# Kernel optimization log

Hardware: AMD Instinct MI355X
Metric: run time of the kernel (lower is better)

Reference implementation:

```python
import jax, jax.numpy as jnp
import numpy as np

N = 20000          # num nodes
E = 320000         # num edges (avg degree 16)
IN = 128           # input feature dim
HID = 64           # layer1 out_channels per head
OUT = 128          # layer2 out_channels per head
H = 3              # attention heads
NEG = 0.15         # LeakyReLU negative slope
IN2 = IN + H * HID # layer2 input: concat(x, h1)


def setup_inputs() -> dict:
    key = jax.random.key(0)
    ks = jax.random.split(key, 12)
    lin = lambda k, fi, fo: (jax.random.normal(k, (fi, fo), jnp.float32) / np.float32(np.sqrt(fi)))
    return {
        "node_features": jax.random.normal(ks[0], (N, IN), jnp.float32),
        "Wl1": lin(ks[1], IN, H * HID),
        "bl1": jnp.zeros((H * HID,), jnp.float32),
        "Wr1": lin(ks[2], IN, H * HID),
        "br1": jnp.zeros((H * HID,), jnp.float32),
        "att1": jax.random.normal(ks[3], (H, HID), jnp.float32) / np.float32(np.sqrt(HID)),
        "bias1": jnp.zeros((H * HID,), jnp.float32),
        "Wl2": lin(ks[4], IN2, H * OUT),
        "bl2": jnp.zeros((H * OUT,), jnp.float32),
        "Wr2": lin(ks[5], IN2, H * OUT),
        "br2": jnp.zeros((H * OUT,), jnp.float32),
        "att2": jax.random.normal(ks[6], (H, OUT), jnp.float32) / np.float32(np.sqrt(OUT)),
        "bias2": jnp.zeros((OUT,), jnp.float32),
        "edge_index": jax.random.randint(ks[7], (2, E), 0, N, jnp.int64),
    }


def _gatv2(x, src, dst, Wl, bl, Wr, br, att, bias, concat):
    """PyG GATv2Conv (add_self_loops=False, eval/no dropout).
    src=edge_index[0] (message source j), dst=edge_index[1] (target i)."""
    n = x.shape[0]
    h, c = att.shape
    xl = (x @ Wl + bl).reshape(n, h, c)   # lin_l -> source/message features
    xr = (x @ Wr + br).reshape(n, h, c)   # lin_r -> target features
    e = xl[src] + xr[dst]                 # [E,H,C]
    e = jnp.where(e > 0, e, NEG * e)      # LeakyReLU
    logits = jnp.einsum('ehc,hc->eh', e, att)  # [E,H]
    # segment softmax over incoming edges of each dst node
    m = jax.ops.segment_max(logits, dst, num_segments=n)
    ex = jnp.exp(logits - m[dst])
    denom = jax.ops.segment_sum(ex, dst, num_segments=n)
    alpha = ex / (denom[dst] + 1e-16)
    out = jax.ops.segment_sum(xl[src] * alpha[:, :, None], dst, num_segments=n)  # [N,H,C]
    if concat:
        return out.reshape(n, h * c) + bias
    return out.mean(axis=1) + bias


def reference(node_features, Wl1, bl1, Wr1, br1, att1, bias1,
              Wl2, bl2, Wr2, br2, att2, bias2, edge_index):
    src, dst = edge_index[0], edge_index[1]
    h1 = jax.nn.relu(_gatv2(node_features, src, dst, Wl1, bl1, Wr1, br1, att1, bias1, True))
    h = jnp.concatenate([node_features, h1], axis=-1)  # [N, IN2]
    h2 = jax.nn.relu(_gatv2(h, src, dst, Wl2, bl2, Wr2, br2, att2, bias2, False))
    return h2
```

## Files before the change

kernel.cpp:

```cpp
#include <hip/hip_runtime.h>
#include <hip/hip_bf16.h>

#define NN 20000
#define EE 320000
#define IN 128
#define HID 64
#define OUTC 128
#define NH 3
#define NEG 0.15f
#define IN2 320
#define HO1 192
#define HO2 384
#define NB_SCAN 79
#define GRIDM128 157
#define LDA 72

typedef __hip_bfloat16 bf16;
typedef __attribute__((ext_vector_type(8))) short short8;
typedef __attribute__((ext_vector_type(4))) float f32x4;

__device__ __forceinline__ float bf2f(bf16 v) { return __bfloat162float(v); }
__device__ __forceinline__ bf16 f2bf(float v) { return __float2bfloat16(v); }
__device__ __forceinline__ float lo16(unsigned int d) {
    union { unsigned int u; float f; } c; c.u = d << 16; return c.f;
}
__device__ __forceinline__ float hi16(unsigned int d) {
    union { unsigned int u; float f; } c; c.u = d & 0xffff0000u; return c.f;
}

__global__ void k_count(const int* __restrict__ ei, int* __restrict__ cnt) {
    const int e = blockIdx.x * 256 + threadIdx.x;
    if (e < EE) atomicAdd(&cnt[ei[EE + e]], 1);
}

__global__ void k_scanA(const int* __restrict__ cnt, int* __restrict__ loc,
                        int* __restrict__ bsum) {
    __shared__ int sh[256];
    const int t = threadIdx.x;
    const int i = blockIdx.x * 256 + t;
    const int v = (i < NN) ? cnt[i] : 0;
    sh[t] = v; __syncthreads();
    for (int off = 1; off < 256; off <<= 1) {
        const int add = (t >= off) ? sh[t - off] : 0;
        __syncthreads();
        sh[t] += add; __syncthreads();
    }
    if (i < NN) loc[i] = sh[t];
    if (t == 255) bsum[blockIdx.x] = sh[255];
}

__global__ void k_scanB(int* __restrict__ bsum) {
    __shared__ int sh[128];
    const int t = threadIdx.x;
    const int v = (t < NB_SCAN) ? bsum[t] : 0;
    sh[t] = v; __syncthreads();
    for (int off = 1; off < 128; off <<= 1) {
        const int add = (t >= off) ? sh[t - off] : 0;
        __syncthreads();
        sh[t] += add; __syncthreads();
    }
    if (t < NB_SCAN) bsum[t] = sh[t] - v;
}

__global__ void k_scanC(const int* __restrict__ loc, const int* __restrict__ cnt,
                        const int* __restrict__ bsum, int* __restrict__ row_off,
                        int* __restrict__ fill) {
    const int i = blockIdx.x * 256 + threadIdx.x;
    if (i < NN) {
        const int ro = loc[i] - cnt[i] + bsum[blockIdx.x];
        row_off[i] = ro; fill[i] = ro;
    }
    if (i == 0) row_off[NN] = EE;
}

__global__ void k_scatter(const int* __restrict__ ei, int* __restrict__ fill,
                          int* __restrict__ csr_src) {
    const int e = blockIdx.x * 256 + threadIdx.x;
    if (e < EE) {
        const int p = atomicAdd(&fill[ei[EE + e]], 1);
        csr_src[p] = ei[e];
    }
}

__global__ void k_a2x(const float* __restrict__ x, bf16* __restrict__ xb) {
    const int idx = blockIdx.x * 256 + threadIdx.x;
    if (idx < NN * IN) xb[idx] = f2bf(x[idx]);
}

__global__ void k_wt(const float* __restrict__ Wl, const float* __restrict__ Wr,
                     int K, int NO, bf16* __restrict__ Wt) {
    const int idx = blockIdx.x * 256 + threadIdx.x;
    if (idx >= 2 * NO * K) return;
    const int n = idx / K, k = idx - n * K;
    const float* W = (n < NO) ? Wl : Wr;
    const int nn = (n < NO) ? n : n - NO;
    Wt[idx] = f2bf(W[(size_t)k * NO + nn]);
}

template <int K, int CH>
__launch_bounds__(256)
__global__ void gemm_mfma(const bf16* __restrict__ A0, int As0,
                          const bf16* __restrict__ A1, int As1,
                          const bf16* __restrict__ Wt,
                          const float* __restrict__ bl, const float* __restrict__ br,
                          int NO, size_t planeN,
                          bf16* __restrict__ outl, bf16* __restrict__ outr) {
    __shared__ bf16 Asm[128 * LDA];
    __shared__ bf16 Bsm[128 * LDA];
    const int tid = threadIdx.x;
    const int w = tid >> 6, lane = tid & 63;
    const int quad = lane >> 4, l15 = lane & 15;
    const int r0 = (w >> 1) * 64;
    const int c0 = (w & 1) * 64;
    const int m0 = blockIdx.x * 128;
    const int n0 = blockIdx.y * 128;

    f32x4 acc[4][4];
#pragma unroll
    for (int nt = 0; nt < 4; ++nt) {
        const int col = n0 + c0 + nt * 16 + l15;
        const float b = (col < NO) ? bl[col] : br[col - NO];
#pragma unroll
        for (int mt = 0; mt < 4; ++mt) acc[mt][nt] = (f32x4){b, b, b, b};
    }

    int arow[4]; size_t boff[4]; int soff[4];
#pragma unroll
    for (int q = 0; q < 4; ++q) {
        const int s = q * 256 + tid;
        int r = m0 + (s >> 3); if (r >= NN) r = NN - 1;
        arow[q] = r;
        boff[q] = (size_t)(n0 + (s >> 3)) * K + (s & 7) * 8;
        soff[q] = (s >> 3) * LDA + (s & 7) * 8;
    }

    short8 pa[4], pb[4];
#pragma unroll
    for (int q = 0; q < 4; ++q) {
        const int s = q * 256 + tid;
        pa[q] = *(const short8*)(A0 + (size_t)arow[q] * As0 + (s & 7) * 8);
        pb[q] = *(const short8*)(Wt + boff[q]);
    }

#pragma unroll
    for (int ks = 0; ks < K; ks += 64) {
#pragma unroll
        for (int q = 0; q < 4; ++q) {
            *(short8*)&Asm[soff[q]] = pa[q];
            *(short8*)&Bsm[soff[q]] = pb[q];
        }
        __syncthreads();
        if (ks + 64 < K) {
            const int nks = ks + 64;
#pragma unroll
            for (int q = 0; q < 4; ++q) {
                const int s = q * 256 + tid;
                const bf16* ap = (K <= 128 || nks < 128)
                    ? (A0 + (size_t)arow[q] * As0 + nks + (s & 7) * 8)
                    : (A1 + (size_t)arow[q] * As1 + (nks - 128) + (s & 7) * 8);
                pa[q] = *(const short8*)ap;
                pb[q] = *(const short8*)(Wt + boff[q] + nks);
            }
        }
#pragma unroll
        for (int kq = 0; kq < 2; ++kq) {
            short8 af[4], bf[4];
#pragma unroll
            for (int mt = 0; mt < 4; ++mt)
                af[mt] = *(const short8*)&Asm[(r0 + mt * 16 + l15) * LDA + kq * 32 + quad * 8];
#pragma unroll
            for (int nt = 0; nt < 4; ++nt)
                bf[nt] = *(const short8*)&Bsm[(c0 + nt * 16 + l15) * LDA + kq * 32 + quad * 8];
#pragma unroll
            for (int mt = 0; mt < 4; ++mt)
#pragma unroll
                for (int nt = 0; nt < 4; ++nt)
                    acc[mt][nt] = __builtin_amdgcn_mfma_f32_16x16x32_bf16(af[mt], bf[nt], acc[mt][nt], 0, 0, 0);
        }
        __syncthreads();
    }

#pragma unroll
    for (int mt = 0; mt < 4; ++mt)
#pragma unroll
    for (int nt = 0; nt < 4; ++nt) {
        const int col = n0 + c0 + nt * 16 + l15;
        const int cc = (col < NO) ? col : col - NO;
        bf16* o = (col < NO) ? outl : outr;
        const int h = cc / CH, c = cc - h * CH;
#pragma unroll
        for (int r = 0; r < 4; ++r) {
            const int row = m0 + r0 + mt * 16 + quad * 4 + r;
            if (row < NN) o[h * planeN + (size_t)row * CH + c] = f2bf(acc[mt][nt][r]);
        }
    }
}

__global__ void gather1(const int* __restrict__ row_off, const int* __restrict__ csr_src,
                        const bf16* __restrict__ xl, const bf16* __restrict__ xr,
                        const float* __restrict__ att, const float* __restrict__ bias,
                        bf16* __restrict__ h1) {
    const int i = blockIdx.x;
    const int w = threadIdx.x >> 6;
    const int lane = threadIdx.x & 63;
    const int g = lane >> 3;
    const int t = lane & 7;
    const unsigned short* xlu = (const unsigned short*)xl + (size_t)w * NN * HID;
    const unsigned short* xru = (const unsigned short*)xr + (size_t)w * NN * HID;
    float rv[8], av1[8], av2[8];
    {
        const uint4 ru = *(const uint4*)(xru + (size_t)i * HID + 8 * t);
        rv[0] = lo16(ru.x); rv[1] = hi16(ru.x);
        rv[2] = lo16(ru.y); rv[3] = hi16(ru.y);
        rv[4] = lo16(ru.z); rv[5] = hi16(ru.z);
        rv[6] = lo16(ru.w); rv[7] = hi16(ru.w);
#pragma unroll
        for (int c = 0; c < 8; ++c) {
            const float a = att[w * HID + 8 * t + c];
            av1[c] = 0.575f * a;
            av2[c] = 0.425f * a;
        }
    }
    float acc[8] = {0.f, 0.f, 0.f, 0.f, 0.f, 0.f, 0.f, 0.f};
    float den = 0.f;
    const int kb = row_off[i], ke = row_off[i + 1];
    if (kb < ke) {
        const int idx0 = kb + g;
        uint4 lu = *(const uint4*)(xlu +
            (size_t)csr_src[idx0 < ke ? idx0 : ke - 1] * HID + 8 * t);
        int jn = 0;
        if (kb + 8 < ke) {
            const int idx1 = kb + 8 + g;
            jn = csr_src[idx1 < ke ? idx1 : ke - 1];
        }
        for (int p0 = kb; p0 < ke; p0 += 8) {
            const bool more = (p0 + 8 < ke);
            uint4 lun;
            if (more) lun = *(const uint4*)(xlu + (size_t)jn * HID + 8 * t);
            if (p0 + 16 < ke) {
                const int idx2 = p0 + 16 + g;
                jn = csr_src[idx2 < ke ? idx2 : ke - 1];
            }
            float lv[8];
            lv[0] = lo16(lu.x); lv[1] = hi16(lu.x);
            lv[2] = lo16(lu.y); lv[3] = hi16(lu.y);
            lv[4] = lo16(lu.z); lv[5] = hi16(lu.z);
            lv[6] = lo16(lu.w); lv[7] = hi16(lu.w);
            float p1 = 0.f, p2 = 0.f;
#pragma unroll
            for (int c = 0; c < 8; ++c) {
                const float s = lv[c] + rv[c];
                p1 = fmaf(av1[c], s, p1);
                p2 = fmaf(av2[c], fabsf(s), p2);
            }
            float p = p1 + p2;
            p += __shfl_xor(p, 1, 64);
            p += __shfl_xor(p, 2, 64);
            p += __shfl_xor(p, 4, 64);
            const int idx = p0 + g;
            const float ex = (idx < ke) ? __expf(p) : 0.f;
#pragma unroll
            for (int c = 0; c < 8; ++c) acc[c] = fmaf(ex, lv[c], acc[c]);
            den += ex;
            if (more) lu = lun;
        }
    }
    __shared__ float part[NH][8][HID];
    __shared__ float dsh[NH][8];
    *(f32x4*)&part[w][g][8 * t]     = (f32x4){acc[0], acc[1], acc[2], acc[3]};
    *(f32x4*)&part[w][g][8 * t + 4] = (f32x4){acc[4], acc[5], acc[6], acc[7]};
    if (t == 0) dsh[w][g] = den;
    __syncthreads();
    const int o = threadIdx.x;
    const int hh = o >> 6, c = o & 63;
    float num = 0.f, dd = 0.f;
#pragma unroll
    for (int q = 0; q < 8; ++q) { num += part[hh][q][c]; dd += dsh[hh][q]; }
    const float v = num / (dd + 1e-16f) + bias[o];
    h1[(size_t)i * HO1 + o] = f2bf(v > 0.f ? v : 0.f);
}

__global__ void gather2(const int* __restrict__ row_off, const int* __restrict__ csr_src,
                        const bf16* __restrict__ xl2, const bf16* __restrict__ xr2,
                        const float* __restrict__ att2, const float* __restrict__ bias2,
                        float* __restrict__ out) {
    const int i = blockIdx.x;
    const int w = threadIdx.x >> 6;
    const int lane = threadIdx.x & 63;
    const int g = lane >> 4;
    const int t = lane & 15;
    const unsigned short* xlu = (const unsigned short*)xl2 + (size_t)w * NN * OUTC;
    const unsigned short* xru = (const unsigned short*)xr2 + (size_t)w * NN * OUTC;
    float rv[8], av1[8], av2[8];
    {
        const uint4 ru = *(const uint4*)(xru + (size_t)i * OUTC + 8 * t);
        rv[0] = lo16(ru.x); rv[1] = hi16(ru.x);
        rv[2] = lo16(ru.y); rv[3] = hi16(ru.y);
        rv[4] = lo16(ru.z); rv[5] = hi16(ru.z);
        rv[6] = lo16(ru.w); rv[7] = hi16(ru.w);
#pragma unroll
        for (int c = 0; c < 8; ++c) {
            const float a = att2[w * OUTC + 8 * t + c];
            av1[c] = 0.575f * a;
            av2[c] = 0.425f * a;
        }
    }
    float acc[8] = {0.f, 0.f, 0.f, 0.f, 0.f, 0.f, 0.f, 0.f};
    float den = 0.f;
    const int kb = row_off[i], ke = row_off[i + 1];
    if (kb < ke) {
        const int idx0 = kb + g;
        uint4 lu = *(const uint4*)(xlu +
            (size_t)csr_src[idx0 < ke ? idx0 : ke - 1] * OUTC + 8 * t);
        int jn = 0;
        if (kb + 4 < ke) {
            const int idx1 = kb + 4 + g;
            jn = csr_src[idx1 < ke ? idx1 : ke - 1];
        }
        for (int p0 = kb; p0 < ke; p0 += 4) {
            const bool more = (p0 + 4 < ke);
            uint4 lun;
            if (more) lun = *(const uint4*)(xlu + (size_t)jn * OUTC + 8 * t);
            if (p0 + 8 < ke) {
                const int idx2 = p0 + 8 + g;
                jn = csr_src[idx2 < ke ? idx2 : ke - 1];
            }
            float lv[8];
            lv[0] = lo16(lu.x); lv[1] = hi16(lu.x);
            lv[2] = lo16(lu.y); lv[3] = hi16(lu.y);
            lv[4] = lo16(lu.z); lv[5] = hi16(lu.z);
            lv[6] = lo16(lu.w); lv[7] = hi16(lu.w);
            float p1 = 0.f, p2 = 0.f;
#pragma unroll
            for (int c = 0; c < 8; ++c) {
                const float s = lv[c] + rv[c];
                p1 = fmaf(av1[c], s, p1);
                p2 = fmaf(av2[c], fabsf(s), p2);
            }
            float p = p1 + p2;
            p += __shfl_xor(p, 1, 64);
            p += __shfl_xor(p, 2, 64);
            p += __shfl_xor(p, 4, 64);
            p += __shfl_xor(p, 8, 64);
            const int idx = p0 + g;
            const float ex = (idx < ke) ? __expf(p) : 0.f;
#pragma unroll
            for (int c = 0; c < 8; ++c) acc[c] = fmaf(ex, lv[c], acc[c]);
            den += ex;
            if (more) lu = lun;
        }
    }
    __shared__ float part[NH][4][OUTC];
    __shared__ float dsh[NH][4];
    *(f32x4*)&part[w][g][8 * t]     = (f32x4){acc[0], acc[1], acc[2], acc[3]};
    *(f32x4*)&part[w][g][8 * t + 4] = (f32x4){acc[4], acc[5], acc[6], acc[7]};
    if (t == 0) dsh[w][g] = den;
    __syncthreads();
    if (threadIdx.x < OUTC) {
        const int c = threadIdx.x;
        float v = 0.f;
#pragma unroll
        for (int hh = 0; hh < NH; ++hh) {
            float num = part[hh][0][c] + part[hh][1][c] + part[hh][2][c] + part[hh][3][c];
            float dd  = dsh[hh][0] + dsh[hh][1] + dsh[hh][2] + dsh[hh][3];
            v += num / (dd + 1e-16f);
        }
        v = v * (1.f / 3.f) + bias2[c];
        out[(size_t)i * OUTC + c] = v > 0.f ? v : 0.f;
    }
}

extern "C" void kernel_launch(void* const* d_in, const int* in_sizes, int n_in,
                              void* d_out, int out_size, void* d_ws, size_t ws_size,
                              hipStream_t stream) {
    const float* x    = (const float*)d_in[0];
    const float* Wl1  = (const float*)d_in[1];
    const float* bl1  = (const float*)d_in[2];
    const float* Wr1  = (const float*)d_in[3];
    const float* br1  = (const float*)d_in[4];
    const float* att1 = (const float*)d_in[5];
    const float* bias1= (const float*)d_in[6];
    const float* Wl2  = (const float*)d_in[7];
    const float* bl2  = (const float*)d_in[8];
    const float* Wr2  = (const float*)d_in[9];
    const float* br2  = (const float*)d_in[10];
    const float* att2 = (const float*)d_in[11];
    const float* bias2= (const float*)d_in[12];
    const int*   ei   = (const int*)d_in[13];

    char* ws = (char*)d_ws;
    bf16*  xb     = (bf16*)(ws);
    bf16*  h1b    = (bf16*)(ws + 5120000);
    bf16*  xl1    = (bf16*)(ws + 12800000);
    bf16*  xr1    = (bf16*)(ws + 20480000);
    bf16*  xl2    = (bf16*)(ws + 12800000);
    bf16*  xr2    = (bf16*)(ws + 28160000);
    int*   cnt    = (int*)(ws + 43520000);
    int*   fill   = (int*)(ws + 43600000);
    int*   loc    = (int*)(ws + 43680000);
    int*   bsum   = (int*)(ws + 43760000);
    int*   rowoff = (int*)(ws + 43764096);
    int*   csrsrc = (int*)(ws + 43844104);
    bf16*  Wt1    = (bf16*)(ws + 45124112);
    bf16*  Wt2    = (bf16*)(ws + 45222416);

    k_a2x<<<(NN * IN + 255) / 256, 256, 0, stream>>>(x, xb);
    k_wt<<<(HO2 * IN + 255) / 256, 256, 0, stream>>>(Wl1, Wr1, IN, HO1, Wt1);
    k_wt<<<(2 * HO2 * IN2 + 255) / 256, 256, 0, stream>>>(Wl2, Wr2, IN2, HO2, Wt2);

    hipMemsetAsync(cnt, 0, NN * sizeof(int), stream);
    k_count<<<(EE + 255) / 256, 256, 0, stream>>>(ei, cnt);
    k_scanA<<<NB_SCAN, 256, 0, stream>>>(cnt, loc, bsum);
    k_scanB<<<1, 128, 0, stream>>>(bsum);
    k_scanC<<<NB_SCAN, 256, 0, stream>>>(loc, cnt, bsum, rowoff, fill);
    k_scatter<<<(EE + 255) / 256, 256, 0, stream>>>(ei, fill, csrsrc);

    gemm_mfma<IN, HID><<<dim3(GRIDM128, HO2 / 128), 256, 0, stream>>>(
        xb, IN, (const bf16*)nullptr, 0, Wt1, bl1, br1, HO1,
        (size_t)NN * HID, xl1, xr1);
    gather1<<<NN, 192, 0, stream>>>(rowoff, csrsrc, xl1, xr1, att1, bias1, h1b);

    gemm_mfma<IN2, OUTC><<<dim3(GRIDM128, 2 * HO2 / 128), 256, 0, stream>>>(
        xb, IN, h1b, HO1, Wt2, bl2, br2, HO2,
        (size_t)NN * OUTC, xl2, xr2);
    gather2<<<NN, 192, 0, stream>>>(rowoff, csrsrc, xl2, xr2, att2, bias2,
                                    (float*)d_out);
}
```

Before: 236.4 us.

## Merge preprocessing and scan kernels, use packed f32 math in gathers

Fuses the input conversion, both weight transposes and the count-zeroing memset into one kernel. It also replaces the three-kernel prefix scan with a single 1024-thread block scan. The gather kernels' inner loops now use v_pk_add_f32 and v_pk_fma_f32 inline asm to cut the count of VALU instructions. Together these remove several launches and their serialization gaps. The risk is that the single-block scan is serial per thread, and that the inline asm may prevent some compiler scheduling.

```diff
diff --git a/kernel.cpp b/kernel.cpp
--- a/kernel.cpp
+++ b/kernel.cpp
@@ -11,13 +11,13 @@
 #define IN2 320
 #define HO1 192
 #define HO2 384
-#define NB_SCAN 79
 #define GRIDM128 157
 #define LDA 72
 
 typedef __hip_bfloat16 bf16;
 typedef __attribute__((ext_vector_type(8))) short short8;
 typedef __attribute__((ext_vector_type(4))) float f32x4;
+typedef __attribute__((ext_vector_type(2))) float f32x2;
 
 __device__ __forceinline__ float bf2f(bf16 v) { return __bfloat162float(v); }
 __device__ __forceinline__ bf16 f2bf(float v) { return __float2bfloat16(v); }
@@ -27,50 +27,50 @@
 __device__ __forceinline__ float hi16(unsigned int d) {
     union { unsigned int u; float f; } c; c.u = d & 0xffff0000u; return c.f;
 }
+__device__ __forceinline__ f32x2 upk(unsigned int d) {
+    f32x2 r; r.x = lo16(d); r.y = hi16(d); return r;
+}
+__device__ __forceinline__ f32x2 pk_add(f32x2 a, f32x2 b) {
+    f32x2 d; asm("v_pk_add_f32 %0, %1, %2" : "=v"(d) : "v"(a), "v"(b)); return d;
+}
+__device__ __forceinline__ f32x2 pk_fma(f32x2 a, f32x2 b, f32x2 c) {
+    f32x2 d; asm("v_pk_fma_f32 %0, %1, %2, %3" : "=v"(d) : "v"(a), "v"(b), "v"(c)); return d;
+}
+__device__ __forceinline__ f32x2 pk_abs(f32x2 a) {
+    union { f32x2 f; unsigned int u[2]; } c; c.f = a;
+    c.u[0] &= 0x7fffffffu; c.u[1] &= 0x7fffffffu; return c.f;
+}
 
 __global__ void k_count(const int* __restrict__ ei, int* __restrict__ cnt) {
     const int e = blockIdx.x * 256 + threadIdx.x;
     if (e < EE) atomicAdd(&cnt[ei[EE + e]], 1);
 }
 
-__global__ void k_scanA(const int* __restrict__ cnt, int* __restrict__ loc,
-                        int* __restrict__ bsum) {
-    __shared__ int sh[256];
+__global__ void k_scan(const int* __restrict__ cnt, int* __restrict__ row_off,
+                       int* __restrict__ fill) {
+    __shared__ int sh[1024];
     const int t = threadIdx.x;
-    const int i = blockIdx.x * 256 + t;
-    const int v = (i < NN) ? cnt[i] : 0;
-    sh[t] = v; __syncthreads();
-    for (int off = 1; off < 256; off <<= 1) {
+    const int i0 = t * 20;
+    int s = 0;
+    if (i0 < NN) {
+#pragma unroll
+        for (int k = 0; k < 20; ++k) s += cnt[i0 + k];
+    }
+    sh[t] = s; __syncthreads();
+    for (int off = 1; off < 1024; off <<= 1) {
         const int add = (t >= off) ? sh[t - off] : 0;
         __syncthreads();
         sh[t] += add; __syncthreads();
     }
-    if (i < NN) loc[i] = sh[t];
-    if (t == 255) bsum[blockIdx.x] = sh[255];
-}
-
-__global__ void k_scanB(int* __restrict__ bsum) {
-    __shared__ int sh[128];
-    const int t = threadIdx.x;
-    const int v = (t < NB_SCAN) ? bsum[t] : 0;
-    sh[t] = v; __syncthreads();
-    for (int off = 1; off < 128; off <<= 1) {
-        const int add = (t >= off) ? sh[t - off] : 0;
-        __syncthreads();
-        sh[t] += add; __syncthreads();
-    }
-    if (t < NB_SCAN) bsum[t] = sh[t] - v;
-}
-
-__global__ void k_scanC(const int* __restrict__ loc, const int* __restrict__ cnt,
-                        const int* __restrict__ bsum, int* __restrict__ row_off,
-                        int* __restrict__ fill) {
-    const int i = blockIdx.x * 256 + threadIdx.x;
-    if (i < NN) {
-        const int ro = loc[i] - cnt[i] + bsum[blockIdx.x];
-        row_off[i] = ro; fill[i] = ro;
-    }
-    if (i == 0) row_off[NN] = EE;
+    int o = t ? sh[t - 1] : 0;
+    if (i0 < NN) {
+        for (int k = 0; k < 20; ++k) {
+            const int idx = i0 + k;
+            row_off[idx] = o; fill[idx] = o;
+            o += cnt[idx];
+        }
+    }
+    if (t == 0) row_off[NN] = EE;
 }
 
 __global__ void k_scatter(const int* __restrict__ ei, int* __restrict__ fill,
@@ -82,19 +82,26 @@
     }
 }
 
-__global__ void k_a2x(const float* __restrict__ x, bf16* __restrict__ xb) {
+__global__ void k_pre(const float* __restrict__ x, bf16* __restrict__ xb,
+                      const float* __restrict__ Wl1, const float* __restrict__ Wr1,
+                      bf16* __restrict__ Wt1,
+                      const float* __restrict__ Wl2, const float* __restrict__ Wr2,
+                      bf16* __restrict__ Wt2, int* __restrict__ cnt) {
     const int idx = blockIdx.x * 256 + threadIdx.x;
     if (idx < NN * IN) xb[idx] = f2bf(x[idx]);
-}
-
-__global__ void k_wt(const float* __restrict__ Wl, const float* __restrict__ Wr,
-                     int K, int NO, bf16* __restrict__ Wt) {
-    const int idx = blockIdx.x * 256 + threadIdx.x;
-    if (idx >= 2 * NO * K) return;
-    const int n = idx / K, k = idx - n * K;
-    const float* W = (n < NO) ? Wl : Wr;
-    const int nn = (n < NO) ? n : n - NO;
-    Wt[idx] = f2bf(W[(size_t)k * NO + nn]);
+    if (idx < 2 * HO1 * IN) {
+        const int n = idx / IN, k = idx - n * IN;
+        const float* W = (n < HO1) ? Wl1 : Wr1;
+        const int nn = (n < HO1) ? n : n - HO1;
+        Wt1[idx] = f2bf(W[(size_t)k * HO1 + nn]);
+    }
+    if (idx < 2 * HO2 * IN2) {
+        const int n = idx / IN2, k = idx - n * IN2;
+        const float* W = (n < HO2) ? Wl2 : Wr2;
+        const int nn = (n < HO2) ? n : n - HO2;
+        Wt2[idx] = f2bf(W[(size_t)k * HO2 + nn]);
+    }
+    if (idx < NN) cnt[idx] = 0;
 }
 
 template <int K, int CH>
@@ -207,21 +214,19 @@
     const int t = lane & 7;
     const unsigned short* xlu = (const unsigned short*)xl + (size_t)w * NN * HID;
     const unsigned short* xru = (const unsigned short*)xr + (size_t)w * NN * HID;
-    float rv[8], av1[8], av2[8];
+    f32x2 rvp[4], av1p[4], av2p[4];
     {
         const uint4 ru = *(const uint4*)(xru + (size_t)i * HID + 8 * t);
-        rv[0] = lo16(ru.x); rv[1] = hi16(ru.x);
-        rv[2] = lo16(ru.y); rv[3] = hi16(ru.y);
-        rv[4] = lo16(ru.z); rv[5] = hi16(ru.z);
-        rv[6] = lo16(ru.w); rv[7] = hi16(ru.w);
-#pragma unroll
-        for (int c = 0; c < 8; ++c) {
-            const float a = att[w * HID + 8 * t + c];
-            av1[c] = 0.575f * a;
-            av2[c] = 0.425f * a;
-        }
-    }
-    float acc[8] = {0.f, 0.f, 0.f, 0.f, 0.f, 0.f, 0.f, 0.f};
+        rvp[0] = upk(ru.x); rvp[1] = upk(ru.y); rvp[2] = upk(ru.z); rvp[3] = upk(ru.w);
+#pragma unroll
+        for (int m = 0; m < 4; ++m) {
+            const float a0 = att[w * HID + 8 * t + 2 * m];
+            const float a1 = att[w * HID + 8 * t + 2 * m + 1];
+            av1p[m] = (f32x2){0.575f * a0, 0.575f * a1};
+            av2p[m] = (f32x2){0.425f * a0, 0.425f * a1};
+        }
+    }
+    f32x2 accp[4] = {(f32x2){0.f, 0.f}, (f32x2){0.f, 0.f}, (f32x2){0.f, 0.f}, (f32x2){0.f, 0.f}};
     float den = 0.f;
     const int kb = row_off[i], ke = row_off[i + 1];
     if (kb < ke) {
@@ -241,34 +246,32 @@
                 const int idx2 = p0 + 16 + g;
                 jn = csr_src[idx2 < ke ? idx2 : ke - 1];
             }
-            float lv[8];
-            lv[0] = lo16(lu.x); lv[1] = hi16(lu.x);
-            lv[2] = lo16(lu.y); lv[3] = hi16(lu.y);
-            lv[4] = lo16(lu.z); lv[5] = hi16(lu.z);
-            lv[6] = lo16(lu.w); lv[7] = hi16(lu.w);
-            float p1 = 0.f, p2 = 0.f;
-#pragma unroll
-            for (int c = 0; c < 8; ++c) {
-                const float s = lv[c] + rv[c];
-                p1 = fmaf(av1[c], s, p1);
-                p2 = fmaf(av2[c], fabsf(s), p2);
+            f32x2 lvp[4];
+            lvp[0] = upk(lu.x); lvp[1] = upk(lu.y); lvp[2] = upk(lu.z); lvp[3] = upk(lu.w);
+            f32x2 p1p = (f32x2){0.f, 0.f}, p2p = (f32x2){0.f, 0.f};
+#pragma unroll
+            for (int m = 0; m < 4; ++m) {
+                const f32x2 s = pk_add(lvp[m], rvp[m]);
+                p1p = pk_fma(av1p[m], s, p1p);
+                p2p = pk_fma(av2p[m], pk_abs(s), p2p);
             }
-            float p = p1 + p2;
+            float p = (p1p.x + p2p.x) + (p1p.y + p2p.y);
             p += __shfl_xor(p, 1, 64);
             p += __shfl_xor(p, 2, 64);
             p += __shfl_xor(p, 4, 64);
             const int idx = p0 + g;
             const float ex = (idx < ke) ? __expf(p) : 0.f;
-#pragma unroll
-            for (int c = 0; c < 8; ++c) acc[c] = fmaf(ex, lv[c], acc[c]);
+            const f32x2 exv = (f32x2){ex, ex};
+#pragma unroll
+            for (int m = 0; m < 4; ++m) accp[m] = pk_fma(lvp[m], exv, accp[m]);
             den += ex;
             if (more) lu = lun;
         }
     }
     __shared__ float part[NH][8][HID];
     __shared__ float dsh[NH][8];
-    *(f32x4*)&part[w][g][8 * t]     = (f32x4){acc[0], acc[1], acc[2], acc[3]};
-    *(f32x4*)&part[w][g][8 * t + 4] = (f32x4){acc[4], acc[5], acc[6], acc[7]};
+    *(f32x4*)&part[w][g][8 * t]     = (f32x4){accp[0].x, accp[0].y, accp[1].x, accp[1].y};
+    *(f32x4*)&part[w][g][8 * t + 4] = (f32x4){accp[2].x, accp[2].y, accp[3].x, accp[3].y};
     if (t == 0) dsh[w][g] = den;
     __syncthreads();
     const int o = threadIdx.x;
@@ -291,21 +294,19 @@
     const int t = lane & 15;
     const unsigned short* xlu = (const unsigned short*)xl2 + (size_t)w * NN * OUTC;
     const unsigned short* xru = (const unsigned short*)xr2 + (size_t)w * NN * OUTC;
-    float rv[8], av1[8], av2[8];
+    f32x2 rvp[4], av1p[4], av2p[4];
     {
         const uint4 ru = *(const uint4*)(xru + (size_t)i * OUTC + 8 * t);
-        rv[0] = lo16(ru.x); rv[1] = hi16(ru.x);
-        rv[2] = lo16(ru.y); rv[3] = hi16(ru.y);
-        rv[4] = lo16(ru.z); rv[5] = hi16(ru.z);
-        rv[6] = lo16(ru.w); rv[7] = hi16(ru.w);
-#pragma unroll
-        for (int c = 0; c < 8; ++c) {
-            const float a = att2[w * OUTC + 8 * t + c];
-            av1[c] = 0.575f * a;
-            av2[c] = 0.425f * a;
-        }
-    }
-    float acc[8] = {0.f, 0.f, 0.f, 0.f, 0.f, 0.f, 0.f, 0.f};
+        rvp[0] = upk(ru.x); rvp[1] = upk(ru.y); rvp[2] = upk(ru.z); rvp[3] = upk(ru.w);
+#pragma unroll
+        for (int m = 0; m < 4; ++m) {
+            const float a0 = att2[w * OUTC + 8 * t + 2 * m];
+            const float a1 = att2[w * OUTC + 8 * t + 2 * m + 1];
+            av1p[m] = (f32x2){0.575f * a0, 0.575f * a1};
+            av2p[m] = (f32x2){0.425f * a0, 0.425f * a1};
+        }
+    }
+    f32x2 accp[4] = {(f32x2){0.f, 0.f}, (f32x2){0.f, 0.f}, (f32x2){0.f, 0.f}, (f32x2){0.f, 0.f}};
     float den = 0.f;
     const int kb = row_off[i], ke = row_off[i + 1];
     if (kb < ke) {
@@ -325,35 +326,33 @@
                 const int idx2 = p0 + 8 + g;
                 jn = csr_src[idx2 < ke ? idx2 : ke - 1];
             }
-            float lv[8];
-            lv[0] = lo16(lu.x); lv[1] = hi16(lu.x);
-            lv[2] = lo16(lu.y); lv[3] = hi16(lu.y);
-            lv[4] = lo16(lu.z); lv[5] = hi16(lu.z);
-            lv[6] = lo16(lu.w); lv[7] = hi16(lu.w);
-            float p1 = 0.f, p2 = 0.f;
-#pragma unroll
-            for (int c = 0; c < 8; ++c) {
-                const float s = lv[c] + rv[c];
-                p1 = fmaf(av1[c], s, p1);
-                p2 = fmaf(av2[c], fabsf(s), p2);
+            f32x2 lvp[4];
+            lvp[0] = upk(lu.x); lvp[1] = upk(lu.y); lvp[2] = upk(lu.z); lvp[3] = upk(lu.w);
+            f32x2 p1p = (f32x2){0.f, 0.f}, p2p = (f32x2){0.f, 0.f};
+#pragma unroll
+            for (int m = 0; m < 4; ++m) {
+                const f32x2 s = pk_add(lvp[m], rvp[m]);
+                p1p = pk_fma(av1p[m], s, p1p);
+                p2p = pk_fma(av2p[m], pk_abs(s), p2p);
             }
-            float p = p1 + p2;
+            float p = (p1p.x + p2p.x) + (p1p.y + p2p.y);
             p += __shfl_xor(p, 1, 64);
             p += __shfl_xor(p, 2, 64);
             p += __shfl_xor(p, 4, 64);
             p += __shfl_xor(p, 8, 64);
             const int idx = p0 + g;
             const float ex = (idx < ke) ? __expf(p) : 0.f;
-#pragma unroll
-            for (int c = 0; c < 8; ++c) acc[c] = fmaf(ex, lv[c], acc[c]);
+            const f32x2 exv = (f32x2){ex, ex};
+#pragma unroll
+            for (int m = 0; m < 4; ++m) accp[m] = pk_fma(lvp[m], exv, accp[m]);
             den += ex;
             if (more) lu = lun;
         }
     }
     __shared__ float part[NH][4][OUTC];
     __shared__ float dsh[NH][4];
-    *(f32x4*)&part[w][g][8 * t]     = (f32x4){acc[0], acc[1], acc[2], acc[3]};
-    *(f32x4*)&part[w][g][8 * t + 4] = (f32x4){acc[4], acc[5], acc[6], acc[7]};
+    *(f32x4*)&part[w][g][8 * t]     = (f32x4){accp[0].x, accp[0].y, accp[1].x, accp[1].y};
+    *(f32x4*)&part[w][g][8 * t + 4] = (f32x4){accp[2].x, accp[2].y, accp[3].x, accp[3].y};
     if (t == 0) dsh[w][g] = den;
     __syncthreads();
     if (threadIdx.x < OUTC) {
@@ -397,22 +396,16 @@
     bf16*  xr2    = (bf16*)(ws + 28160000);
     int*   cnt    = (int*)(ws + 43520000);
     int*   fill   = (int*)(ws + 43600000);
-    int*   loc    = (int*)(ws + 43680000);
-    int*   bsum   = (int*)(ws + 43760000);
     int*   rowoff = (int*)(ws + 43764096);
     int*   csrsrc = (int*)(ws + 43844104);
     bf16*  Wt1    = (bf16*)(ws + 45124112);
     bf16*  Wt2    = (bf16*)(ws + 45222416);
 
-    k_a2x<<<(NN * IN + 255) / 256, 256, 0, stream>>>(x, xb);
-    k_wt<<<(HO2 * IN + 255) / 256, 256, 0, stream>>>(Wl1, Wr1, IN, HO1, Wt1);
-    k_wt<<<(2 * HO2 * IN2 + 255) / 256, 256, 0, stream>>>(Wl2, Wr2, IN2, HO2, Wt2);
-
-    hipMemsetAsync(cnt, 0, NN * sizeof(int), stream);
+    k_pre<<<(NN * IN + 255) / 256, 256, 0, stream>>>(
+        x, xb, Wl1, Wr1, Wt1, Wl2, Wr2, Wt2, cnt);
+
     k_count<<<(EE + 255) / 256, 256, 0, stream>>>(ei, cnt);
-    k_scanA<<<NB_SCAN, 256, 0, stream>>>(cnt, loc, bsum);
-    k_scanB<<<1, 128, 0, stream>>>(bsum);
-    k_scanC<<<NB_SCAN, 256, 0, stream>>>(loc, cnt, bsum, rowoff, fill);
+    k_scan<<<1, 1024, 0, stream>>>(cnt, rowoff, fill);
     k_scatter<<<(EE + 255) / 256, 256, 0, stream>>>(ei, fill, csrsrc);
 
     gemm_mfma<IN, HID><<<dim3(GRIDM128, HO2 / 128), 256, 0, stream>>>(
```

After: 234.0 us. About the same (-1.0%).
